# Kernel tuning notes

Hardware: AMD Instinct MI355X
Metric: run time of the kernel (lower is better)

The kernel has to match this reference:

```python
import jax, jax.numpy as jnp
import numpy as np

N_MOL = 128      # molecules per batch (per side)
ATOMS = 32       # atoms per molecule
N_AT = N_MOL * ATOMS
DIM = 64
NFP = 10000
LAYER_HIDDEN = 3
LAYER_OUTPUT = 2
DESC = 55
FEAT = 2 * DIM + 59  # 187


def _block_diag_adj(k, seg):
    # random dense adjacency masked to the block-diagonal structure produced by pad()
    a = jax.random.uniform(k, (N_AT, N_AT), dtype=jnp.float32)
    mask = (seg[:, None] == seg[None, :]).astype(jnp.float32)
    return a * mask


def setup_inputs() -> dict:
    key = jax.random.key(0)
    ks = jax.random.split(key, 24)
    seg = jnp.repeat(jnp.arange(N_MOL), ATOMS)  # molecule id per atom (sorted)
    inp = {
        'adj_D': _block_diag_adj(ks[0], seg),
        'adj_A': _block_diag_adj(ks[1], seg),
        'fp_D': jax.random.randint(ks[2], (N_AT,), 0, NFP),
        'fp_A': jax.random.randint(ks[3], (N_AT,), 0, NFP),
        'seg_D': seg,
        'seg_A': seg,
        'homo_D': jax.random.normal(ks[4], (N_MOL, 1), dtype=jnp.float32),
        'lumo_D': jax.random.normal(ks[5], (N_MOL, 1), dtype=jnp.float32),
        'homo_A': jax.random.normal(ks[6], (N_MOL, 1), dtype=jnp.float32),
        'lumo_A': jax.random.normal(ks[7], (N_MOL, 1), dtype=jnp.float32),
        'descriptors': jax.random.normal(ks[8], (N_MOL, DESC), dtype=jnp.float32),
        'correct_values': jax.random.normal(ks[9], (N_MOL, 1), dtype=jnp.float32),
        'embed': jax.random.normal(ks[10], (NFP, DIM), dtype=jnp.float32),
        'Wf_w': jax.random.normal(ks[11], (LAYER_HIDDEN, DIM, DIM), dtype=jnp.float32) * (1.0 / np.sqrt(DIM)),
        'Wf_b': jax.random.normal(ks[12], (LAYER_HIDDEN, DIM), dtype=jnp.float32) * 0.01,
        'Wo_w': jax.random.normal(ks[13], (LAYER_OUTPUT, FEAT, FEAT), dtype=jnp.float32) * (1.0 / np.sqrt(FEAT)),
        'Wo_b': jax.random.normal(ks[14], (LAYER_OUTPUT, FEAT), dtype=jnp.float32) * 0.01,
        'Wp_w': jax.random.normal(ks[15], (1, FEAT), dtype=jnp.float32) * (1.0 / np.sqrt(FEAT)),
        'Wp_b': jax.random.normal(ks[16], (1,), dtype=jnp.float32) * 0.01,
    }
    return inp


def _l2norm(h):
    # torch F.normalize(h, 2, 1): x / max(||x||_2, eps)
    n = jnp.sqrt(jnp.sum(h * h, axis=1, keepdims=True))
    return h / jnp.maximum(n, 1e-12)


def _gnn_side(adj, v, Wf_w, Wf_b):
    for l in range(LAYER_HIDDEN):
        h = jax.nn.relu(v @ Wf_w[l].T + Wf_b[l])  # [N_AT, DIM]
        v = _l2norm(h + adj @ h)                   # residual + block-diag message passing
    return v


def reference(adj_D, adj_A, fp_D, fp_A, seg_D, seg_A,
              homo_D, lumo_D, homo_A, lumo_A, descriptors, correct_values,
              embed, Wf_w, Wf_b, Wo_w, Wo_b, Wp_w, Wp_b):
    v_D = embed[fp_D]
    v_A = embed[fp_A]
    v_D = _gnn_side(adj_D, v_D, Wf_w, Wf_b)
    v_A = _gnn_side(adj_A, v_A, Wf_w, Wf_b)
    mol_D = jax.ops.segment_sum(v_D, seg_D, num_segments=N_MOL)  # sum-pool per molecule
    mol_A = jax.ops.segment_sum(v_A, seg_A, num_segments=N_MOL)
    x = jnp.concatenate([mol_D, homo_D, lumo_D, mol_A, homo_A, lumo_A, descriptors], axis=1)  # [N_MOL, 187]
    for l in range(LAYER_OUTPUT):
        x = jax.nn.relu(x @ Wo_w[l].T + Wo_b[l])
    pred = x @ Wp_w.T + Wp_b  # [N_MOL, 1]
    loss = jnp.mean((pred - correct_values) ** 2)
    return loss
```

## Files before the change

### kernel.cpp

```cpp
#include <hip/hip_runtime.h>

#define N_MOL 128
#define ATOMS 32
#define N_AT  4096
#define DIM   64
#define FEAT  187

__global__ __launch_bounds__(512) void gnn_kernel(
    const float* __restrict__ adj_D, const float* __restrict__ adj_A,
    const int*   __restrict__ fp_D,  const int*   __restrict__ fp_A,
    const float* __restrict__ embed,
    const float* __restrict__ Wf_w,  const float* __restrict__ Wf_b,
    float* __restrict__ mol_out )
{
    __shared__ float v_s[ATOMS][DIM];
    __shared__ float h_s[ATOMS][DIM];
    __shared__ float adj_s[ATOMS][ATOMS];
    __shared__ float w_s[DIM][DIM];
    __shared__ float b_s[DIM];

    const int blk  = blockIdx.x;
    const int side = blk >> 7;
    const int m    = blk & 127;
    const float* adj = side ? adj_A : adj_D;
    const int*   fp  = side ? fp_A  : fp_D;

    const int tid = threadIdx.x;

    for (int i = tid; i < ATOMS * ATOMS; i += 512) {
        int r = i >> 5, c = i & 31;
        adj_s[r][c] = adj[(size_t)(m * ATOMS + r) * N_AT + (m * ATOMS + c)];
    }
    for (int i = tid; i < ATOMS * DIM; i += 512) {
        int a = i >> 6, d = i & 63;
        v_s[a][d] = embed[(size_t)fp[m * ATOMS + a] * DIM + d];
    }

    const int a  = tid >> 4;
    const int d0 = (tid & 15) * 4;

    for (int l = 0; l < 3; ++l) {
        for (int i = tid; i < DIM * DIM; i += 512)
            ((float*)w_s)[i] = Wf_w[l * DIM * DIM + i];
        if (tid < DIM) b_s[tid] = Wf_b[l * DIM + tid];
        __syncthreads();

        float acc[4];
        #pragma unroll
        for (int j = 0; j < 4; ++j) acc[j] = b_s[d0 + j];
        for (int k = 0; k < DIM; ++k) {
            float vk = v_s[a][k];
            #pragma unroll
            for (int j = 0; j < 4; ++j) acc[j] += vk * w_s[d0 + j][k];
        }
        #pragma unroll
        for (int j = 0; j < 4; ++j) h_s[a][d0 + j] = fmaxf(acc[j], 0.0f);
        __syncthreads();

        float t[4];
        #pragma unroll
        for (int j = 0; j < 4; ++j) t[j] = h_s[a][d0 + j];
        for (int b = 0; b < ATOMS; ++b) {
            float ab = adj_s[a][b];
            #pragma unroll
            for (int j = 0; j < 4; ++j) t[j] += ab * h_s[b][d0 + j];
        }
        float ss = t[0]*t[0] + t[1]*t[1] + t[2]*t[2] + t[3]*t[3];
        #pragma unroll
        for (int msk = 1; msk < 16; msk <<= 1)
            ss += __shfl_xor(ss, msk);
        float scale = 1.0f / fmaxf(sqrtf(ss), 1e-12f);
        #pragma unroll
        for (int j = 0; j < 4; ++j) v_s[a][d0 + j] = t[j] * scale;
        __syncthreads();
    }

    if (tid < DIM) {
        float s = 0.0f;
        for (int aa = 0; aa < ATOMS; ++aa) s += v_s[aa][tid];
        mol_out[(size_t)side * N_MOL * DIM + m * DIM + tid] = s;
    }
}

__global__ __launch_bounds__(256) void head_kernel(
    const float* __restrict__ mol,
    const float* __restrict__ homo_D, const float* __restrict__ lumo_D,
    const float* __restrict__ homo_A, const float* __restrict__ lumo_A,
    const float* __restrict__ desc,   const float* __restrict__ cv,
    const float* __restrict__ Wo_w,   const float* __restrict__ Wo_b,
    const float* __restrict__ Wp_w,   const float* __restrict__ Wp_b,
    float* __restrict__ sq_out )
{
    __shared__ float x_s[FEAT];
    __shared__ float y_s[FEAT];
    __shared__ float red_s[256];

    const int m = blockIdx.x;
    const int t = threadIdx.x;

    if (t < 64) x_s[t] = mol[m * DIM + t];
    if (t >= 64 && t < 128) x_s[66 + (t - 64)] = mol[N_MOL * DIM + m * DIM + (t - 64)];
    if (t >= 128 && t < 183) x_s[132 + (t - 128)] = desc[m * 55 + (t - 128)];
    if (t == 183) x_s[64]  = homo_D[m];
    if (t == 184) x_s[65]  = lumo_D[m];
    if (t == 185) x_s[130] = homo_A[m];
    if (t == 186) x_s[131] = lumo_A[m];
    __syncthreads();

    float* xin  = x_s;
    float* xout = y_s;
    for (int l = 0; l < 2; ++l) {
        float acc = 0.0f;
        if (t < FEAT) {
            acc = Wo_b[l * FEAT + t];
            const float* wr = Wo_w + ((size_t)l * FEAT + t) * FEAT;
            for (int k = 0; k < FEAT; ++k) acc += xin[k] * wr[k];
            acc = fmaxf(acc, 0.0f);
        }
        __syncthreads();
        if (t < FEAT) xout[t] = acc;
        __syncthreads();
        float* tmp = xin; xin = xout; xout = tmp;
    }

    red_s[t] = (t < FEAT) ? xin[t] * Wp_w[t] : 0.0f;
    __syncthreads();
    for (int s = 128; s > 0; s >>= 1) {
        if (t < s) red_s[t] += red_s[t + s];
        __syncthreads();
    }
    if (t == 0) {
        float pred = red_s[0] + Wp_b[0];
        float d = pred - cv[m];
        sq_out[m] = d * d;
    }
}

__global__ __launch_bounds__(64) void loss_kernel(
    const float* __restrict__ sq, float* __restrict__ out)
{
    const int t = threadIdx.x;
    float v = sq[t] + sq[t + 64];
    #pragma unroll
    for (int msk = 32; msk >= 1; msk >>= 1)
        v += __shfl_xor(v, msk);
    if (t == 0) out[0] = v * (1.0f / 128.0f);
}

extern "C" void kernel_launch(void* const* d_in, const int* in_sizes, int n_in,
                              void* d_out, int out_size, void* d_ws, size_t ws_size,
                              hipStream_t stream) {
    const float* adj_D  = (const float*)d_in[0];
    const float* adj_A  = (const float*)d_in[1];
    const int*   fp_D   = (const int*)  d_in[2];
    const int*   fp_A   = (const int*)  d_in[3];
    const float* homo_D = (const float*)d_in[6];
    const float* lumo_D = (const float*)d_in[7];
    const float* homo_A = (const float*)d_in[8];
    const float* lumo_A = (const float*)d_in[9];
    const float* desc   = (const float*)d_in[10];
    const float* cv     = (const float*)d_in[11];
    const float* embed  = (const float*)d_in[12];
    const float* Wf_w   = (const float*)d_in[13];
    const float* Wf_b   = (const float*)d_in[14];
    const float* Wo_w   = (const float*)d_in[15];
    const float* Wo_b   = (const float*)d_in[16];
    const float* Wp_w   = (const float*)d_in[17];
    const float* Wp_b   = (const float*)d_in[18];

    float* ws  = (float*)d_ws;
    float* mol = ws;
    float* sq  = ws + 2 * N_MOL * DIM;

    gnn_kernel<<<256, 512, 0, stream>>>(adj_D, adj_A, fp_D, fp_A, embed,
                                        Wf_w, Wf_b, mol);
    head_kernel<<<N_MOL, 256, 0, stream>>>(mol, homo_D, lumo_D, homo_A, lumo_A,
                                           desc, cv, Wo_w, Wo_b, Wp_w, Wp_b, sq);
    loss_kernel<<<1, 64, 0, stream>>>(sq, (float*)d_out);
}
```

Measured before the change: 215.5 us.

## Preload all GNN weights transposed and swizzled in LDS, vectorize shared accesses

The GNN kernel now loads all three layer weight matrices once, transposed with an XOR swizzle, so the inner matmul can read float4 weight rows without bank conflicts and drops the per-layer weight reload and its barrier. Adjacency, embedding and activation traffic uses float4 loads and stores, with padded shared arrays to avoid bank conflicts. The head kernel's dot product is manually unrolled by four to break the serial dependency chain. The cost is more LDS per block (about 60KB), which may lower occupancy.

Result: faster. 200.2 us (-7.1%).

```diff
diff --git a/kernel.cpp b/kernel.cpp
--- a/kernel.cpp
+++ b/kernel.cpp
@@ -5,6 +5,8 @@
 #define N_AT  4096
 #define DIM   64
 #define FEAT  187
+#define PADV  68
+#define PADA  33
 
 __global__ __launch_bounds__(512) void gnn_kernel(
     const float* __restrict__ adj_D, const float* __restrict__ adj_A,
@@ -13,70 +15,99 @@
     const float* __restrict__ Wf_w,  const float* __restrict__ Wf_b,
     float* __restrict__ mol_out )
 {
-    __shared__ float v_s[ATOMS][DIM];
-    __shared__ float h_s[ATOMS][DIM];
-    __shared__ float adj_s[ATOMS][ATOMS];
-    __shared__ float w_s[DIM][DIM];
-    __shared__ float b_s[DIM];
+    __shared__ float wT_s[3][DIM][DIM];
+    __shared__ float b_s[3][DIM];
+    __shared__ float v_s[ATOMS][PADV];
+    __shared__ float h_s[ATOMS][PADV];
+    __shared__ float adj_s[ATOMS][PADA];
 
     const int blk  = blockIdx.x;
     const int side = blk >> 7;
     const int m    = blk & 127;
     const float* adj = side ? adj_A : adj_D;
     const int*   fp  = side ? fp_A  : fp_D;
-
     const int tid = threadIdx.x;
 
-    for (int i = tid; i < ATOMS * ATOMS; i += 512) {
-        int r = i >> 5, c = i & 31;
-        adj_s[r][c] = adj[(size_t)(m * ATOMS + r) * N_AT + (m * ATOMS + c)];
-    }
-    for (int i = tid; i < ATOMS * DIM; i += 512) {
-        int a = i >> 6, d = i & 63;
-        v_s[a][d] = embed[(size_t)fp[m * ATOMS + a] * DIM + d];
-    }
+    for (int i4 = tid; i4 < 3 * DIM * DIM / 4; i4 += 512) {
+        float4 w = ((const float4*)Wf_w)[i4];
+        int i  = i4 << 2;
+        int l  = i >> 12;
+        int d  = (i >> 6) & 63;
+        int k0 = i & 63;
+        const float* wp = (const float*)&w;
+        #pragma unroll
+        for (int kk = 0; kk < 4; ++kk) {
+            int k  = k0 + kk;
+            int dg = (d >> 2) ^ (k & 15);
+            wT_s[l][k][(dg << 2) + (d & 3)] = wp[kk];
+        }
+    }
+    if (tid < 3 * DIM) ((float*)b_s)[tid] = Wf_b[tid];
+
+    for (int i4 = tid; i4 < ATOMS * ATOMS / 4; i4 += 512) {
+        int r  = i4 >> 3;
+        int c4 = (i4 & 7) << 2;
+        float4 av = *(const float4*)&adj[(size_t)(m * ATOMS + r) * N_AT + m * ATOMS + c4];
+        adj_s[r][c4 + 0] = av.x; adj_s[r][c4 + 1] = av.y;
+        adj_s[r][c4 + 2] = av.z; adj_s[r][c4 + 3] = av.w;
+    }
+    {
+        int a  = tid >> 4;
+        int d4 = (tid & 15) << 2;
+        float4 ev = *(const float4*)&embed[(size_t)fp[m * ATOMS + a] * DIM + d4];
+        *(float4*)&v_s[a][d4] = ev;
+    }
+    __syncthreads();
 
     const int a  = tid >> 4;
-    const int d0 = (tid & 15) * 4;
+    const int g  = tid & 15;
+    const int d0 = g << 2;
 
     for (int l = 0; l < 3; ++l) {
-        for (int i = tid; i < DIM * DIM; i += 512)
-            ((float*)w_s)[i] = Wf_w[l * DIM * DIM + i];
-        if (tid < DIM) b_s[tid] = Wf_b[l * DIM + tid];
-        __syncthreads();
-
-        float acc[4];
+        float accv[4];
+        *(float4*)accv = *(const float4*)&b_s[l][d0];
+        const float* vrow = v_s[a];
         #pragma unroll
-        for (int j = 0; j < 4; ++j) acc[j] = b_s[d0 + j];
-        for (int k = 0; k < DIM; ++k) {
-            float vk = v_s[a][k];
+        for (int k0 = 0; k0 < DIM; k0 += 4) {
+            float4 vv = *(const float4*)&vrow[k0];
+            const float* vp = (const float*)&vv;
             #pragma unroll
-            for (int j = 0; j < 4; ++j) acc[j] += vk * w_s[d0 + j][k];
-        }
-        #pragma unroll
-        for (int j = 0; j < 4; ++j) h_s[a][d0 + j] = fmaxf(acc[j], 0.0f);
-        __syncthreads();
-
-        float t[4];
-        #pragma unroll
-        for (int j = 0; j < 4; ++j) t[j] = h_s[a][d0 + j];
+            for (int kk = 0; kk < 4; ++kk) {
+                int k = k0 + kk;
+                float4 ww = *(const float4*)&wT_s[l][k][(g ^ (k & 15)) << 2];
+                float vs = vp[kk];
+                accv[0] += vs * ww.x; accv[1] += vs * ww.y;
+                accv[2] += vs * ww.z; accv[3] += vs * ww.w;
+            }
+        }
+        float4 hst;
+        hst.x = fmaxf(accv[0], 0.0f); hst.y = fmaxf(accv[1], 0.0f);
+        hst.z = fmaxf(accv[2], 0.0f); hst.w = fmaxf(accv[3], 0.0f);
+        *(float4*)&h_s[a][d0] = hst;
+        __syncthreads();
+
+        float4 tv = *(const float4*)&h_s[a][d0];
+        float t0 = tv.x, t1 = tv.y, t2 = tv.z, t3 = tv.w;
+        const float* arow = adj_s[a];
+        #pragma unroll 8
         for (int b = 0; b < ATOMS; ++b) {
-            float ab = adj_s[a][b];
-            #pragma unroll
-            for (int j = 0; j < 4; ++j) t[j] += ab * h_s[b][d0 + j];
-        }
-        float ss = t[0]*t[0] + t[1]*t[1] + t[2]*t[2] + t[3]*t[3];
+            float ab = arow[b];
+            float4 hb = *(const float4*)&h_s[b][d0];
+            t0 += ab * hb.x; t1 += ab * hb.y; t2 += ab * hb.z; t3 += ab * hb.w;
+        }
+        float ss = t0 * t0 + t1 * t1 + t2 * t2 + t3 * t3;
         #pragma unroll
         for (int msk = 1; msk < 16; msk <<= 1)
             ss += __shfl_xor(ss, msk);
         float scale = 1.0f / fmaxf(sqrtf(ss), 1e-12f);
-        #pragma unroll
-        for (int j = 0; j < 4; ++j) v_s[a][d0 + j] = t[j] * scale;
+        float4 sv; sv.x = t0 * scale; sv.y = t1 * scale; sv.z = t2 * scale; sv.w = t3 * scale;
+        *(float4*)&v_s[a][d0] = sv;
         __syncthreads();
     }
 
     if (tid < DIM) {
         float s = 0.0f;
+        #pragma unroll 8
         for (int aa = 0; aa < ATOMS; ++aa) s += v_s[aa][tid];
         mol_out[(size_t)side * N_MOL * DIM + m * DIM + tid] = s;
     }
@@ -91,8 +122,8 @@
     const float* __restrict__ Wp_w,   const float* __restrict__ Wp_b,
     float* __restrict__ sq_out )
 {
-    __shared__ float x_s[FEAT];
-    __shared__ float y_s[FEAT];
+    __shared__ float x_s[FEAT + 1];
+    __shared__ float y_s[FEAT + 1];
     __shared__ float red_s[256];
 
     const int m = blockIdx.x;
@@ -114,7 +145,13 @@
         if (t < FEAT) {
             acc = Wo_b[l * FEAT + t];
             const float* wr = Wo_w + ((size_t)l * FEAT + t) * FEAT;
-            for (int k = 0; k < FEAT; ++k) acc += xin[k] * wr[k];
+            int k = 0;
+            #pragma unroll 1
+            for (; k < 184; k += 4) {
+                acc += xin[k] * wr[k] + xin[k+1] * wr[k+1]
+                     + xin[k+2] * wr[k+2] + xin[k+3] * wr[k+3];
+            }
+            acc += xin[184] * wr[184] + xin[185] * wr[185] + xin[186] * wr[186];
             acc = fmaxf(acc, 0.0f);
         }
         __syncthreads();
```
